# Kernel optimization log

Hardware: AMD Instinct MI355X
Metric: run time of the kernel (lower is better)

## Reference

```python
import jax, jax.numpy as jnp
import numpy as np
from jax import lax

M_RANGE = 1  # padding = m_range, kernel is (2*m_range+1)^2 = 9 classes of 3x3


def _conv(x, kernel):
    # torch F.conv2d (cross-correlation), stride 1, padding M_RANGE
    return lax.conv_general_dilated(
        x, kernel, window_strides=(1, 1),
        padding=[(M_RANGE, M_RANGE), (M_RANGE, M_RANGE)],
        dimension_numbers=('NCHW', 'OIHW', 'NCHW'))


def _construct_seg(ones, m_mask, m_kernel):
    # ones.expand_as(m_mask) * m_mask, then per-sample conv2d -> batched conv
    return _conv(ones * m_mask, m_kernel)  # [B,1,H,W]


def _construct_image(im, m_mask, appear, m_kernel):
    # im: [B,C,H,W]; m_mask: [B,K,H,W]; appear: [B,1,H,W]
    im = im * appear
    B, C, H, W = im.shape
    K = m_mask.shape[1]
    # fuse the python double loop: fold (B,C) into batch, conv K->1 once
    im_expand = (im[:, :, None, :, :] * m_mask[:, None, :, :, :]).reshape(B * C, K, H, W)
    return _conv(im_expand, m_kernel).reshape(B, C, H, W)


def setup_inputs() -> dict:
    key = jax.random.key(0)
    k0, k1, k2, k3 = jax.random.split(key, 4)
    B, C, H, W, K, N_INPUTS = 32, 3, 256, 256, 9, 2
    im_input_f = jax.random.uniform(k0, (B, N_INPUTS * C, H, W), dtype=jnp.float32)
    im_input_b = jax.random.uniform(k1, (B, N_INPUTS * C, H, W), dtype=jnp.float32)
    ones = jnp.ones((B, 1, H, W), dtype=jnp.float32)
    # gt motion masks: soft per-pixel distribution over K motion classes
    gt_motion_f = jax.nn.softmax(jax.random.normal(k2, (B, K, H, W), dtype=jnp.float32), axis=1)
    gt_motion_b = jax.nn.softmax(jax.random.normal(k3, (B, K, H, W), dtype=jnp.float32), axis=1)
    # one-hot displacement kernels: kernel i has a 1 at flat position i of the 3x3 window
    m_kernel = jnp.eye(K, dtype=jnp.float32).reshape(K, 3, 3)[None]  # [1,K,3,3]
    return {"im_input_f": im_input_f, "im_input_b": im_input_b, "ones": ones,
            "gt_motion_f": gt_motion_f, "gt_motion_b": gt_motion_b, "m_kernel": m_kernel}


def reference(im_input_f, im_input_b, ones, gt_motion_f, gt_motion_b, m_kernel):
    IM_CHANNEL = 3
    relu = jax.nn.relu
    m_mask_f, m_mask_b = gt_motion_f, gt_motion_b

    seg_f = _construct_seg(ones, m_mask_f, m_kernel)
    seg_b = _construct_seg(ones, m_mask_b, m_kernel)

    disappear_f = relu(seg_f - 1)
    appear_f = relu(1 - disappear_f)
    disappear_b = relu(seg_b - 1)
    appear_b = relu(1 - disappear_b)

    pred_f = _construct_image(im_input_f[:, -IM_CHANNEL:, :, :], m_mask_f, appear_f, m_kernel)
    pred_b = _construct_image(im_input_b[:, -IM_CHANNEL:, :, :], m_mask_b, appear_b, m_kernel)

    seg_f = 1 - relu(1 - seg_f)
    seg_b = 1 - relu(1 - seg_b)
    attn = (seg_f + 1e-5) / (seg_f + seg_b + 2e-5)  # [B,1,H,W], broadcasts over C
    pred = attn * pred_f + (1 - attn) * pred_b
    return (pred, m_mask_f, 1 - appear_f, attn, m_mask_b, 1 - appear_b, 1 - attn)
```

## Files before the change

### kernel.cpp

```cpp
#include <hip/hip_runtime.h>

#define BB 32
#define KK 9
#define CC 3
#define HH 256
#define WW 256
#define HW (HH * WW)
#define NPIX (BB * HW)

#define SZ_P ((size_t)BB * CC * HW)
#define SZ_M ((size_t)BB * KK * HW)
#define SZ_S ((size_t)BB * HW)

__global__ __launch_bounds__(256) void seg_attn_kernel(
    const float* __restrict__ gt_f, const float* __restrict__ gt_b,
    float* __restrict__ out) {
  int idx = blockIdx.x * blockDim.x + threadIdx.x;
  if (idx >= NPIX) return;
  int b  = idx >> 16;
  int hw = idx & (HW - 1);
  int h  = hw >> 8;
  int w  = hw & (WW - 1);

  const float* gf = gt_f + (size_t)b * KK * HW;
  const float* gb = gt_b + (size_t)b * KK * HW;

  float seg_f = 0.f, seg_b = 0.f;
#pragma unroll
  for (int k = 0; k < KK; ++k) {
    int y = h + (k / 3) - 1;
    int x = w + (k % 3) - 1;
    if (y >= 0 && y < HH && x >= 0 && x < WW) {
      int off = k * HW + (y << 8) + x;
      seg_f += gf[off];
      seg_b += gb[off];
    }
  }

  float dis_f = fmaxf(seg_f - 1.f, 0.f);
  float app_f = fmaxf(1.f - dis_f, 0.f);
  float dis_b = fmaxf(seg_b - 1.f, 0.f);
  float app_b = fmaxf(1.f - dis_b, 0.f);
  float sfc = 1.f - fmaxf(1.f - seg_f, 0.f);
  float sbc = 1.f - fmaxf(1.f - seg_b, 0.f);
  float attn = (sfc + 1e-5f) / (sfc + sbc + 2e-5f);

  float* o_disf   = out + SZ_P + SZ_M;
  float* o_attn   = out + SZ_P + SZ_M + SZ_S;
  float* o_disb   = out + SZ_P + 2 * SZ_M + 2 * SZ_S;
  float* o_1mattn = out + SZ_P + 2 * SZ_M + 3 * SZ_S;

  o_disf[idx]   = 1.f - app_f;
  o_attn[idx]   = attn;
  o_disb[idx]   = 1.f - app_b;
  o_1mattn[idx] = 1.f - attn;
}

__global__ __launch_bounds__(256) void pred_kernel(
    const float* __restrict__ im_f, const float* __restrict__ im_b,
    const float* __restrict__ gt_f, const float* __restrict__ gt_b,
    float* __restrict__ out) {
  int idx = blockIdx.x * blockDim.x + threadIdx.x;
  if (idx >= NPIX) return;
  int b  = idx >> 16;
  int hw = idx & (HW - 1);
  int h  = hw >> 8;
  int w  = hw & (WW - 1);

  const float* o_disf = out + SZ_P + SZ_M;
  const float* o_attn = out + SZ_P + SZ_M + SZ_S;
  const float* o_disb = out + SZ_P + 2 * SZ_M + 2 * SZ_S;

  const float* gf  = gt_f + (size_t)b * KK * HW;
  const float* gb  = gt_b + (size_t)b * KK * HW;
  const float* imf = im_f + ((size_t)b * 6 + 3) * HW;
  const float* imb = im_b + ((size_t)b * 6 + 3) * HW;
  const float* dfb = o_disf + (size_t)b * HW;
  const float* dbb = o_disb + (size_t)b * HW;

  float attn = o_attn[idx];

  float pf0 = 0.f, pf1 = 0.f, pf2 = 0.f;
  float pb0 = 0.f, pb1 = 0.f, pb2 = 0.f;
#pragma unroll
  for (int k = 0; k < KK; ++k) {
    int y = h + (k / 3) - 1;
    int x = w + (k % 3) - 1;
    if (y >= 0 && y < HH && x >= 0 && x < WW) {
      int p = (y << 8) + x;
      float af = 1.f - dfb[p];
      float cf = af * gf[k * HW + p];
      pf0 = fmaf(cf, imf[p], pf0);
      pf1 = fmaf(cf, imf[HW + p], pf1);
      pf2 = fmaf(cf, imf[2 * HW + p], pf2);
      float ab = 1.f - dbb[p];
      float cb = ab * gb[k * HW + p];
      pb0 = fmaf(cb, imb[p], pb0);
      pb1 = fmaf(cb, imb[HW + p], pb1);
      pb2 = fmaf(cb, imb[2 * HW + p], pb2);
    }
  }

  float at2 = 1.f - attn;
  size_t base = (size_t)b * CC * HW + hw;
  out[base]          = attn * pf0 + at2 * pb0;
  out[base + HW]     = attn * pf1 + at2 * pb1;
  out[base + 2 * HW] = attn * pf2 + at2 * pb2;
}

extern "C" void kernel_launch(void* const* d_in, const int* in_sizes, int n_in,
                              void* d_out, int out_size, void* d_ws, size_t ws_size,
                              hipStream_t stream) {
  const float* im_f = (const float*)d_in[0];
  const float* im_b = (const float*)d_in[1];
  const float* gt_f = (const float*)d_in[3];
  const float* gt_b = (const float*)d_in[4];
  float* out = (float*)d_out;

  dim3 block(256);
  dim3 grid(NPIX / 256);

  hipMemcpyAsync(out + SZ_P, gt_f, SZ_M * sizeof(float),
                 hipMemcpyDeviceToDevice, stream);
  hipMemcpyAsync(out + SZ_P + SZ_M + 2 * SZ_S, gt_b, SZ_M * sizeof(float),
                 hipMemcpyDeviceToDevice, stream);

  seg_attn_kernel<<<grid, block, 0, stream>>>(gt_f, gt_b, out);
  pred_kernel<<<grid, block, 0, stream>>>(im_f, im_b, gt_f, gt_b, out);
}
```

Before: 446.0 us.

## Fuse seg, attention, mask copy and prediction into one tiled kernel

Replaces the two device-to-device memcpys and two kernels with a single kernel over 32x8 tiles. Each block computes seg sums for its tile plus a one-pixel halo into shared memory, then writes the disappear and attention outputs, copies the mask channels, and computes the prediction using the shared seg values instead of re-reading the stored disappear maps from global memory. This removes an intermediate round-trip through global memory and two launches and copies. In exchange, halo pixels recompute their 9-tap sums redundantly, and the mask copy becomes per-thread scattered stores.

```diff
diff --git a/kernel.cpp b/kernel.cpp
--- a/kernel.cpp
+++ b/kernel.cpp
@@ -6,106 +6,115 @@
 #define HH 256
 #define WW 256
 #define HW (HH * WW)
-#define NPIX (BB * HW)
+#define TW 32
+#define TH 8
+#define HALO_W (TW + 2)
+#define HALO_H (TH + 2)
+#define HALO_N (HALO_W * HALO_H)
 
 #define SZ_P ((size_t)BB * CC * HW)
 #define SZ_M ((size_t)BB * KK * HW)
 #define SZ_S ((size_t)BB * HW)
 
-__global__ __launch_bounds__(256) void seg_attn_kernel(
+__device__ __forceinline__ float clamp01(float v) {
+  return fminf(fmaxf(v, 0.f), 1.f);
+}
+
+__global__ __launch_bounds__(256) void binet_fused_kernel(
+    const float* __restrict__ im_f, const float* __restrict__ im_b,
     const float* __restrict__ gt_f, const float* __restrict__ gt_b,
     float* __restrict__ out) {
-  int idx = blockIdx.x * blockDim.x + threadIdx.x;
-  if (idx >= NPIX) return;
-  int b  = idx >> 16;
-  int hw = idx & (HW - 1);
-  int h  = hw >> 8;
-  int w  = hw & (WW - 1);
+  __shared__ float sf[HALO_H][HALO_W];
+  __shared__ float sb[HALO_H][HALO_W];
+
+  const int tx = threadIdx.x;
+  const int ty = threadIdx.y;
+  const int tid = ty * TW + tx;
+  const int x0 = blockIdx.x * TW;
+  const int y0 = blockIdx.y * TH;
+  const int b  = blockIdx.z;
 
   const float* gf = gt_f + (size_t)b * KK * HW;
   const float* gb = gt_b + (size_t)b * KK * HW;
 
-  float seg_f = 0.f, seg_b = 0.f;
+  for (int i = tid; i < HALO_N; i += TW * TH) {
+    int hy = i / HALO_W;
+    int hx = i - hy * HALO_W;
+    int y = y0 + hy - 1;
+    int x = x0 + hx - 1;
+    float segf = 0.f, segb = 0.f;
+    if (y >= 0 && y < HH && x >= 0 && x < WW) {
+#pragma unroll
+      for (int k = 0; k < KK; ++k) {
+        int yy = y + (k / 3) - 1;
+        int xx = x + (k % 3) - 1;
+        if (yy >= 0 && yy < HH && xx >= 0 && xx < WW) {
+          int off = k * HW + (yy << 8) + xx;
+          segf += gf[off];
+          segb += gb[off];
+        }
+      }
+    }
+    sf[hy][hx] = segf;
+    sb[hy][hx] = segb;
+  }
+  __syncthreads();
+
+  const int x = x0 + tx;
+  const int y = y0 + ty;
+  const int p = (y << 8) + x;
+  const size_t idx = (size_t)b * HW + p;
+
+  float seg_fc = sf[ty + 1][tx + 1];
+  float seg_bc = sb[ty + 1][tx + 1];
+
+  float sfc = fminf(seg_fc, 1.f);
+  float sbc = fminf(seg_bc, 1.f);
+  float attn = (sfc + 1e-5f) / (sfc + sbc + 2e-5f);
+  out[SZ_P + SZ_M + idx]                     = clamp01(seg_fc - 1.f);
+  out[SZ_P + SZ_M + SZ_S + idx]              = attn;
+  out[SZ_P + 2 * SZ_M + 2 * SZ_S + idx]      = clamp01(seg_bc - 1.f);
+  out[SZ_P + 2 * SZ_M + 3 * SZ_S + idx]      = 1.f - attn;
+
+  float* omf = out + SZ_P + (size_t)b * KK * HW + p;
+  float* omb = out + SZ_P + SZ_M + 2 * SZ_S + (size_t)b * KK * HW + p;
 #pragma unroll
   for (int k = 0; k < KK; ++k) {
-    int y = h + (k / 3) - 1;
-    int x = w + (k % 3) - 1;
-    if (y >= 0 && y < HH && x >= 0 && x < WW) {
-      int off = k * HW + (y << 8) + x;
-      seg_f += gf[off];
-      seg_b += gb[off];
-    }
+    omf[(size_t)k * HW] = gf[k * HW + p];
+    omb[(size_t)k * HW] = gb[k * HW + p];
   }
 
-  float dis_f = fmaxf(seg_f - 1.f, 0.f);
-  float app_f = fmaxf(1.f - dis_f, 0.f);
-  float dis_b = fmaxf(seg_b - 1.f, 0.f);
-  float app_b = fmaxf(1.f - dis_b, 0.f);
-  float sfc = 1.f - fmaxf(1.f - seg_f, 0.f);
-  float sbc = 1.f - fmaxf(1.f - seg_b, 0.f);
-  float attn = (sfc + 1e-5f) / (sfc + sbc + 2e-5f);
-
-  float* o_disf   = out + SZ_P + SZ_M;
-  float* o_attn   = out + SZ_P + SZ_M + SZ_S;
-  float* o_disb   = out + SZ_P + 2 * SZ_M + 2 * SZ_S;
-  float* o_1mattn = out + SZ_P + 2 * SZ_M + 3 * SZ_S;
-
-  o_disf[idx]   = 1.f - app_f;
-  o_attn[idx]   = attn;
-  o_disb[idx]   = 1.f - app_b;
-  o_1mattn[idx] = 1.f - attn;
-}
-
-__global__ __launch_bounds__(256) void pred_kernel(
-    const float* __restrict__ im_f, const float* __restrict__ im_b,
-    const float* __restrict__ gt_f, const float* __restrict__ gt_b,
-    float* __restrict__ out) {
-  int idx = blockIdx.x * blockDim.x + threadIdx.x;
-  if (idx >= NPIX) return;
-  int b  = idx >> 16;
-  int hw = idx & (HW - 1);
-  int h  = hw >> 8;
-  int w  = hw & (WW - 1);
-
-  const float* o_disf = out + SZ_P + SZ_M;
-  const float* o_attn = out + SZ_P + SZ_M + SZ_S;
-  const float* o_disb = out + SZ_P + 2 * SZ_M + 2 * SZ_S;
-
-  const float* gf  = gt_f + (size_t)b * KK * HW;
-  const float* gb  = gt_b + (size_t)b * KK * HW;
   const float* imf = im_f + ((size_t)b * 6 + 3) * HW;
   const float* imb = im_b + ((size_t)b * 6 + 3) * HW;
-  const float* dfb = o_disf + (size_t)b * HW;
-  const float* dbb = o_disb + (size_t)b * HW;
-
-  float attn = o_attn[idx];
 
   float pf0 = 0.f, pf1 = 0.f, pf2 = 0.f;
   float pb0 = 0.f, pb1 = 0.f, pb2 = 0.f;
 #pragma unroll
   for (int k = 0; k < KK; ++k) {
-    int y = h + (k / 3) - 1;
-    int x = w + (k % 3) - 1;
-    if (y >= 0 && y < HH && x >= 0 && x < WW) {
-      int p = (y << 8) + x;
-      float af = 1.f - dfb[p];
-      float cf = af * gf[k * HW + p];
-      pf0 = fmaf(cf, imf[p], pf0);
-      pf1 = fmaf(cf, imf[HW + p], pf1);
-      pf2 = fmaf(cf, imf[2 * HW + p], pf2);
-      float ab = 1.f - dbb[p];
-      float cb = ab * gb[k * HW + p];
-      pb0 = fmaf(cb, imb[p], pb0);
-      pb1 = fmaf(cb, imb[HW + p], pb1);
-      pb2 = fmaf(cb, imb[2 * HW + p], pb2);
+    int dy = (k / 3) - 1;
+    int dx = (k % 3) - 1;
+    int yy = y + dy;
+    int xx = x + dx;
+    if (yy >= 0 && yy < HH && xx >= 0 && xx < WW) {
+      int q = (yy << 8) + xx;
+      float af = clamp01(2.f - sf[ty + 1 + dy][tx + 1 + dx]);
+      float wf = af * gf[k * HW + q];
+      pf0 = fmaf(wf, imf[q], pf0);
+      pf1 = fmaf(wf, imf[HW + q], pf1);
+      pf2 = fmaf(wf, imf[2 * HW + q], pf2);
+      float ab = clamp01(2.f - sb[ty + 1 + dy][tx + 1 + dx]);
+      float wb = ab * gb[k * HW + q];
+      pb0 = fmaf(wb, imb[q], pb0);
+      pb1 = fmaf(wb, imb[HW + q], pb1);
+      pb2 = fmaf(wb, imb[2 * HW + q], pb2);
     }
   }
 
   float at2 = 1.f - attn;
-  size_t base = (size_t)b * CC * HW + hw;
-  out[base]          = attn * pf0 + at2 * pb0;
-  out[base + HW]     = attn * pf1 + at2 * pb1;
-  out[base + 2 * HW] = attn * pf2 + at2 * pb2;
+  size_t pbase = (size_t)b * CC * HW + p;
+  out[pbase]          = fmaf(attn, pf0, at2 * pb0);
+  out[pbase + HW]     = fmaf(attn, pf1, at2 * pb1);
+  out[pbase + 2 * HW] = fmaf(attn, pf2, at2 * pb2);
 }
 
 extern "C" void kernel_launch(void* const* d_in, const int* in_sizes, int n_in,
@@ -117,14 +126,7 @@
   const float* gt_b = (const float*)d_in[4];
   float* out = (float*)d_out;
 
-  dim3 block(256);
-  dim3 grid(NPIX / 256);
-
-  hipMemcpyAsync(out + SZ_P, gt_f, SZ_M * sizeof(float),
-                 hipMemcpyDeviceToDevice, stream);
-  hipMemcpyAsync(out + SZ_P + SZ_M + 2 * SZ_S, gt_b, SZ_M * sizeof(float),
-                 hipMemcpyDeviceToDevice, stream);
-
-  seg_attn_kernel<<<grid, block, 0, stream>>>(gt_f, gt_b, out);
-  pred_kernel<<<grid, block, 0, stream>>>(im_f, im_b, gt_f, gt_b, out);
+  dim3 block(TW, TH);
+  dim3 grid(WW / TW, HH / TH, BB);
+  binet_fused_kernel<<<grid, block, 0, stream>>>(im_f, im_b, gt_f, gt_b, out);
 }
```

Measured after the change: 454.3 us. About the same (+1.9%).
